# Optimization experiments

Hardware: AMD Instinct MI355X
Metric: run time of the kernel (lower is better)

The kernel has to match this reference:

```python
import jax, jax.numpy as jnp
import numpy as np

NEG_SLOPE = 0.01  # torch F.leaky_relu default

def leaky_relu(z):
    return jnp.where(z >= 0, z, NEG_SLOPE * z)

def setup_inputs() -> dict:
    key = jax.random.key(0)
    k1, k2, k3, k4, k5, k6, k7 = jax.random.split(key, 7)
    n_nodes, d_feat, n_edges, d_edge = 100000, 64, 1000000, 32
    input_dim, hidden_dim = 2 * d_feat + d_edge, 128
    x = jax.random.normal(k1, (n_nodes, d_feat), dtype=jnp.float32)
    edge_index = jax.random.randint(k2, (2, n_edges), 0, n_nodes, dtype=jnp.int64)
    edge_features = jax.random.normal(k3, (n_edges, d_edge), dtype=jnp.float32)
    lim1 = 1.0 / np.sqrt(input_dim)
    W1 = jax.random.uniform(k4, (hidden_dim, input_dim), minval=-lim1, maxval=lim1, dtype=jnp.float32)
    b1 = jax.random.uniform(k5, (hidden_dim,), minval=-lim1, maxval=lim1, dtype=jnp.float32)
    lim2 = 1.0 / np.sqrt(hidden_dim)
    W2 = jax.random.uniform(k6, (1, hidden_dim), minval=-lim2, maxval=lim2, dtype=jnp.float32)
    b2 = jax.random.uniform(k7, (1,), minval=-lim2, maxval=lim2, dtype=jnp.float32)
    return {"x": x, "edge_index": edge_index, "edge_features": edge_features,
            "W1": W1, "b1": b1, "W2": W2, "b2": b2}

def reference(x, edge_index, edge_features, W1, b1, W2, b2):
    origin, destination = edge_index[0], edge_index[1]
    # gather node features per edge and concat: [E, 2*d_feat + d_edge]
    z = jnp.concatenate([x[origin], x[destination], edge_features], axis=1)
    z = leaky_relu(z @ W1.T + b1)   # [E, hidden]
    z = leaky_relu(z @ W2.T + b2)   # [E, 1]
    return z.reshape(-1)
```

## Files before the change

### kernel.cpp

```cpp
#include <hip/hip_runtime.h>
#include <hip/hip_bf16.h>

typedef __attribute__((ext_vector_type(8)))  short          bf16x8;
typedef __attribute__((ext_vector_type(8)))  unsigned short us8;
typedef __attribute__((ext_vector_type(4)))  unsigned short us4;
typedef __attribute__((ext_vector_type(16))) float          f32x16;

static __device__ __forceinline__ unsigned short f2bf(float f) {
    union { float f; unsigned int u; } v; v.f = f;
    unsigned int u = v.u;
    unsigned int r = u + 0x7fffu + ((u >> 16) & 1u);
    return (unsigned short)(r >> 16);
}

static __device__ __forceinline__ bf16x8 pack8(float4 a, float4 b) {
    bf16x8 r;
    r[0] = (short)f2bf(a.x); r[1] = (short)f2bf(a.y);
    r[2] = (short)f2bf(a.z); r[3] = (short)f2bf(a.w);
    r[4] = (short)f2bf(b.x); r[5] = (short)f2bf(b.y);
    r[6] = (short)f2bf(b.z); r[7] = (short)f2bf(b.w);
    return r;
}

__global__ __launch_bounds__(256) void prep_kernel(
    const float* __restrict__ W1, const float* __restrict__ x,
    unsigned short* __restrict__ w1b, unsigned short* __restrict__ xb,
    int nx, int do_x)
{
    if (blockIdx.x == 0) {
        for (int i = threadIdx.x; i < 128 * 160; i += 256)
            w1b[i] = f2bf(W1[i]);
    } else if (do_x) {
        int n4 = nx >> 2;
        int idx = (blockIdx.x - 1) * 256 + threadIdx.x;
        int stride = (gridDim.x - 1) * 256;
        for (int i = idx; i < n4; i += stride) {
            float4 f = ((const float4*)x)[i];
            us4 o = { f2bf(f.x), f2bf(f.y), f2bf(f.z), f2bf(f.w) };
            ((us4*)xb)[i] = o;
        }
    }
}

template <bool XB>
__global__ __launch_bounds__(256) void edge_mlp(
    const float* __restrict__ x, const unsigned short* __restrict__ xb,
    const int* __restrict__ ei, const float* __restrict__ ef,
    const unsigned short* __restrict__ w1b,
    const float* __restrict__ b1, const float* __restrict__ w2,
    const float* __restrict__ b2, float* __restrict__ out, int E)
{
    __shared__ unsigned short W1s[128][168];
    __shared__ float b1s[128];
    __shared__ float w2s[128];

    const int t = threadIdx.x;
    {
        int j = t >> 1, h = t & 1;
        const unsigned short* src = w1b + j * 160 + h * 80;
        unsigned short* dst = &W1s[j][h * 80];
        #pragma unroll
        for (int i = 0; i < 10; i++)
            *(us8*)(dst + i * 8) = *(const us8*)(src + i * 8);
    }
    if (t < 128) { b1s[t] = b1[t]; w2s[t] = w2[t]; }
    __syncthreads();

    const int lane = t & 63;
    const int wv   = t >> 6;
    const int m    = lane & 31;
    const int kg   = lane >> 5;
    const float b2v = b2[0];

    long e = (long)blockIdx.x * 128 + wv * 32 + m;
    int eidx = (int)((e < (long)E) ? e : (long)(E - 1));
    int o = ei[eidx];
    int d = ei[(size_t)E + eidx];

    bf16x8 afrag[10];
    if constexpr (XB) {
        const bf16x8* xo = (const bf16x8*)(xb + (size_t)o * 64 + kg * 8);
        const bf16x8* xd = (const bf16x8*)(xb + (size_t)d * 64 + kg * 8);
        #pragma unroll
        for (int ks = 0; ks < 4; ks++) afrag[ks]     = xo[ks * 2];
        #pragma unroll
        for (int ks = 0; ks < 4; ks++) afrag[4 + ks] = xd[ks * 2];
    } else {
        const float4* xo = (const float4*)(x + (size_t)o * 64 + kg * 8);
        const float4* xd = (const float4*)(x + (size_t)d * 64 + kg * 8);
        #pragma unroll
        for (int ks = 0; ks < 4; ks++) afrag[ks]     = pack8(xo[ks * 4], xo[ks * 4 + 1]);
        #pragma unroll
        for (int ks = 0; ks < 4; ks++) afrag[4 + ks] = pack8(xd[ks * 4], xd[ks * 4 + 1]);
    }
    {
        const float4* pef = (const float4*)(ef + (size_t)eidx * 32 + kg * 8);
        #pragma unroll
        for (int ks = 0; ks < 2; ks++)
            afrag[8 + ks] = pack8(pef[ks * 4], pef[ks * 4 + 1]);
    }

    f32x16 acc[4];
    #pragma unroll
    for (int i = 0; i < 4; i++)
        #pragma unroll
        for (int r = 0; r < 16; r++) acc[i][r] = 0.0f;

    #pragma unroll
    for (int ks = 0; ks < 10; ks++) {
        const int kb = ks * 16 + kg * 8;
        #pragma unroll
        for (int nt = 0; nt < 4; nt++) {
            bf16x8 bfr = *(const bf16x8*)&W1s[nt * 32 + m][kb];
            acc[nt] = __builtin_amdgcn_mfma_f32_32x32x16_bf16(afrag[ks], bfr, acc[nt], 0, 0, 0);
        }
    }

    const int c = m;
    float b1v[4], w2v[4];
    #pragma unroll
    for (int nt = 0; nt < 4; nt++) {
        b1v[nt] = b1s[nt * 32 + c];
        w2v[nt] = w2s[nt * 32 + c];
    }
    float s[16];
    #pragma unroll
    for (int r = 0; r < 16; r++) {
        float a = 0.0f;
        #pragma unroll
        for (int nt = 0; nt < 4; nt++) {
            float h = acc[nt][r] + b1v[nt];
            h = fmaxf(h, 0.01f * h);
            a = fmaf(h, w2v[nt], a);
        }
        s[r] = a;
    }

    #pragma unroll
    for (int k = 0; k < 4; k++) {
        const int msk = 1 << k;
        const int bit = (c >> k) & 1;
        #pragma unroll
        for (int j = 0; j < (8 >> k); j++) {
            float a0 = s[2 * j], a1 = s[2 * j + 1];
            float keep = bit ? a1 : a0;
            float send = bit ? a0 : a1;
            s[j] = keep + __shfl_xor(send, msk, 64);
        }
    }
    float tot = s[0] + __shfl_xor(s[0], 16, 64);

    if ((c & 16) == 0) {
        int row = (c & 3) + 4 * kg + 8 * ((c >> 2) & 3);
        long oidx = (long)blockIdx.x * 128 + wv * 32 + row;
        if (oidx < (long)E) {
            float v = tot + b2v;
            out[oidx] = fmaxf(v, 0.01f * v);
        }
    }
}

extern "C" void kernel_launch(void* const* d_in, const int* in_sizes, int n_in,
                              void* d_out, int out_size, void* d_ws, size_t ws_size,
                              hipStream_t stream)
{
    const float* x  = (const float*)d_in[0];
    const int*   ei = (const int*)d_in[1];
    const float* ef = (const float*)d_in[2];
    const float* W1 = (const float*)d_in[3];
    const float* b1 = (const float*)d_in[4];
    const float* w2 = (const float*)d_in[5];
    const float* b2 = (const float*)d_in[6];
    float* out = (float*)d_out;

    const int E  = in_sizes[1] / 2;
    const int nx = in_sizes[0];

    unsigned short* w1b = (unsigned short*)d_ws;
    unsigned short* xb  = (unsigned short*)((char*)d_ws + 65536);
    const bool use_xb = ws_size >= (size_t)65536 + (size_t)nx * 2;

    const int nblk = (E + 127) / 128;
    prep_kernel<<<use_xb ? 2048 : 1, 256, 0, stream>>>(W1, x, w1b, xb, nx, use_xb ? 1 : 0);
    if (use_xb)
        edge_mlp<true><<<nblk, 256, 0, stream>>>(x, xb, ei, ef, w1b, b1, w2, b2, out, E);
    else
        edge_mlp<false><<<nblk, 256, 0, stream>>>(x, xb, ei, ef, w1b, b1, w2, b2, out, E);
}
```

Baseline: 284.2 us.

## Use persistent grid-stride edge kernel with software-pipelined gathers

Replaces the one-tile-per-block edge MLP with a persistent kernel of 768 blocks that loop over 128-edge tiles. The next tile's node and edge-feature gathers are issued between MFMAs of the current tile, and indices are prefetched two tiles ahead. This is meant to hide gather latency and to amortise the W1 load into shared memory across many tiles. The trade-off is higher register pressure under the launch_bounds(256,3) occupancy target, and a fixed grid size that may not match every CU count.

```diff
diff --git a/kernel.cpp b/kernel.cpp
--- a/kernel.cpp
+++ b/kernel.cpp
@@ -42,9 +42,21 @@
     }
 }
 
-template <bool XB>
-__global__ __launch_bounds__(256) void edge_mlp(
-    const float* __restrict__ x, const unsigned short* __restrict__ xb,
+#define MFMA4(AF, KS)                                                              \
+    {                                                                              \
+        const int kb_ = (KS) * 16 + kg * 8;                                        \
+        acc[0] = __builtin_amdgcn_mfma_f32_32x32x16_bf16(                          \
+            (AF), *(const bf16x8*)&W1s[0 * 32 + m][kb_], acc[0], 0, 0, 0);         \
+        acc[1] = __builtin_amdgcn_mfma_f32_32x32x16_bf16(                          \
+            (AF), *(const bf16x8*)&W1s[1 * 32 + m][kb_], acc[1], 0, 0, 0);         \
+        acc[2] = __builtin_amdgcn_mfma_f32_32x32x16_bf16(                          \
+            (AF), *(const bf16x8*)&W1s[2 * 32 + m][kb_], acc[2], 0, 0, 0);         \
+        acc[3] = __builtin_amdgcn_mfma_f32_32x32x16_bf16(                          \
+            (AF), *(const bf16x8*)&W1s[3 * 32 + m][kb_], acc[3], 0, 0, 0);         \
+    }
+
+__global__ __launch_bounds__(256, 3) void edge_mlp_pers(
+    const unsigned short* __restrict__ xb,
     const int* __restrict__ ei, const float* __restrict__ ef,
     const unsigned short* __restrict__ w1b,
     const float* __restrict__ b1, const float* __restrict__ w2,
@@ -54,6 +66,145 @@
     __shared__ float b1s[128];
     __shared__ float w2s[128];
 
+    const int tid = threadIdx.x;
+    {
+        int j = tid >> 1, h = tid & 1;
+        const unsigned short* src = w1b + j * 160 + h * 80;
+        unsigned short* dst = &W1s[j][h * 80];
+        #pragma unroll
+        for (int i = 0; i < 10; i++)
+            *(us8*)(dst + i * 8) = *(const us8*)(src + i * 8);
+    }
+    if (tid < 128) { b1s[tid] = b1[tid]; w2s[tid] = w2[tid]; }
+    __syncthreads();
+
+    const int lane = tid & 63;
+    const int wv   = tid >> 6;
+    const int m    = lane & 31;
+    const int kg   = lane >> 5;
+    const float b2v = b2[0];
+    const int laneoff = wv * 32 + m;
+
+    float b1v[4], w2v[4];
+    #pragma unroll
+    for (int nt = 0; nt < 4; nt++) {
+        b1v[nt] = b1s[nt * 32 + m];
+        w2v[nt] = w2s[nt * 32 + m];
+    }
+
+    const int ntiles = (E + 127) >> 7;
+    const int NT = gridDim.x;
+    int t = blockIdx.x;
+    if (t >= ntiles) return;
+
+    auto eclamp = [&](int tt) -> int {
+        if (tt >= ntiles) tt = ntiles - 1;
+        long e = (long)tt * 128 + laneoff;
+        return (int)(e < (long)E ? e : (long)(E - 1));
+    };
+
+    const unsigned short* xk = xb + kg * 8;
+
+    int eA = eclamp(t);
+    int oA = ei[eA], dA = ei[(size_t)E + eA];
+    int eB = eclamp(t + NT);
+    int oB = ei[eB], dB = ei[(size_t)E + eB];
+
+    bf16x8 xo[4], xd[4];
+    float4 efr[4];
+    {
+        const bf16x8* po = (const bf16x8*)(xk + (size_t)oA * 64);
+        const bf16x8* pd = (const bf16x8*)(xk + (size_t)dA * 64);
+        #pragma unroll
+        for (int ks = 0; ks < 4; ks++) { xo[ks] = po[ks * 2]; xd[ks] = pd[ks * 2]; }
+        const float4* pe = (const float4*)(ef + (size_t)eA * 32 + kg * 8);
+        efr[0] = pe[0]; efr[1] = pe[1]; efr[2] = pe[4]; efr[3] = pe[5];
+    }
+
+    while (true) {
+        bf16x8 af8 = pack8(efr[0], efr[1]);
+        bf16x8 af9 = pack8(efr[2], efr[3]);
+
+        int eC = eclamp(t + 2 * NT);
+        int oC = ei[eC], dC = ei[(size_t)E + eC];
+
+        f32x16 acc[4];
+        #pragma unroll
+        for (int i = 0; i < 4; i++)
+            #pragma unroll
+            for (int r = 0; r < 16; r++) acc[i][r] = 0.0f;
+
+        const bf16x8* po = (const bf16x8*)(xk + (size_t)oB * 64);
+        const bf16x8* pd = (const bf16x8*)(xk + (size_t)dB * 64);
+        const float4* pe = (const float4*)(ef + (size_t)eB * 32 + kg * 8);
+
+        #pragma unroll
+        for (int ks = 0; ks < 4; ks++) {
+            MFMA4(xo[ks], ks);
+            xo[ks] = po[ks * 2];
+        }
+        #pragma unroll
+        for (int ks = 0; ks < 4; ks++) {
+            MFMA4(xd[ks], ks + 4);
+            xd[ks] = pd[ks * 2];
+        }
+        MFMA4(af8, 8);
+        efr[0] = pe[0]; efr[1] = pe[1];
+        MFMA4(af9, 9);
+        efr[2] = pe[4]; efr[3] = pe[5];
+
+        float s[16];
+        #pragma unroll
+        for (int r = 0; r < 16; r++) {
+            float a = 0.0f;
+            #pragma unroll
+            for (int nt = 0; nt < 4; nt++) {
+                float h = acc[nt][r] + b1v[nt];
+                h = fmaxf(h, 0.01f * h);
+                a = fmaf(h, w2v[nt], a);
+            }
+            s[r] = a;
+        }
+        #pragma unroll
+        for (int k = 0; k < 4; k++) {
+            const int msk = 1 << k;
+            const int bit = (m >> k) & 1;
+            #pragma unroll
+            for (int j = 0; j < (8 >> k); j++) {
+                float a0 = s[2 * j], a1 = s[2 * j + 1];
+                float keep = bit ? a1 : a0;
+                float send = bit ? a0 : a1;
+                s[j] = keep + __shfl_xor(send, msk, 64);
+            }
+        }
+        float tot = s[0] + __shfl_xor(s[0], 16, 64);
+
+        if ((m & 16) == 0) {
+            int row = (m & 3) + 4 * kg + 8 * ((m >> 2) & 3);
+            long oidx = (long)t * 128 + wv * 32 + row;
+            if (oidx < (long)E) {
+                float v = tot + b2v;
+                out[oidx] = fmaxf(v, 0.01f * v);
+            }
+        }
+
+        t += NT;
+        if (t >= ntiles) break;
+        oB = oC; dB = dC; eB = eC;
+    }
+}
+
+__global__ __launch_bounds__(256) void edge_mlp_fb(
+    const float* __restrict__ x,
+    const int* __restrict__ ei, const float* __restrict__ ef,
+    const unsigned short* __restrict__ w1b,
+    const float* __restrict__ b1, const float* __restrict__ w2,
+    const float* __restrict__ b2, float* __restrict__ out, int E)
+{
+    __shared__ unsigned short W1s[128][168];
+    __shared__ float b1s[128];
+    __shared__ float w2s[128];
+
     const int t = threadIdx.x;
     {
         int j = t >> 1, h = t & 1;
@@ -78,22 +229,13 @@
     int d = ei[(size_t)E + eidx];
 
     bf16x8 afrag[10];
-    if constexpr (XB) {
-        const bf16x8* xo = (const bf16x8*)(xb + (size_t)o * 64 + kg * 8);
-        const bf16x8* xd = (const bf16x8*)(xb + (size_t)d * 64 + kg * 8);
-        #pragma unroll
-        for (int ks = 0; ks < 4; ks++) afrag[ks]     = xo[ks * 2];
-        #pragma unroll
-        for (int ks = 0; ks < 4; ks++) afrag[4 + ks] = xd[ks * 2];
-    } else {
+    {
         const float4* xo = (const float4*)(x + (size_t)o * 64 + kg * 8);
         const float4* xd = (const float4*)(x + (size_t)d * 64 + kg * 8);
         #pragma unroll
         for (int ks = 0; ks < 4; ks++) afrag[ks]     = pack8(xo[ks * 4], xo[ks * 4 + 1]);
         #pragma unroll
         for (int ks = 0; ks < 4; ks++) afrag[4 + ks] = pack8(xd[ks * 4], xd[ks * 4 + 1]);
-    }
-    {
         const float4* pef = (const float4*)(ef + (size_t)eidx * 32 + kg * 8);
         #pragma unroll
         for (int ks = 0; ks < 2; ks++)
@@ -108,20 +250,14 @@
 
     #pragma unroll
     for (int ks = 0; ks < 10; ks++) {
-        const int kb = ks * 16 + kg * 8;
-        #pragma unroll
-        for (int nt = 0; nt < 4; nt++) {
-            bf16x8 bfr = *(const bf16x8*)&W1s[nt * 32 + m][kb];
-            acc[nt] = __builtin_amdgcn_mfma_f32_32x32x16_bf16(afrag[ks], bfr, acc[nt], 0, 0, 0);
-        }
-    }
-
-    const int c = m;
+        MFMA4(afrag[ks], ks);
+    }
+
     float b1v[4], w2v[4];
     #pragma unroll
     for (int nt = 0; nt < 4; nt++) {
-        b1v[nt] = b1s[nt * 32 + c];
-        w2v[nt] = w2s[nt * 32 + c];
+        b1v[nt] = b1s[nt * 32 + m];
+        w2v[nt] = w2s[nt * 32 + m];
     }
     float s[16];
     #pragma unroll
@@ -135,11 +271,10 @@
         }
         s[r] = a;
     }
-
     #pragma unroll
     for (int k = 0; k < 4; k++) {
         const int msk = 1 << k;
-        const int bit = (c >> k) & 1;
+        const int bit = (m >> k) & 1;
         #pragma unroll
         for (int j = 0; j < (8 >> k); j++) {
             float a0 = s[2 * j], a1 = s[2 * j + 1];
@@ -150,8 +285,8 @@
     }
     float tot = s[0] + __shfl_xor(s[0], 16, 64);
 
-    if ((c & 16) == 0) {
-        int row = (c & 3) + 4 * kg + 8 * ((c >> 2) & 3);
+    if ((m & 16) == 0) {
+        int row = (m & 3) + 4 * kg + 8 * ((m >> 2) & 3);
         long oidx = (long)blockIdx.x * 128 + wv * 32 + row;
         if (oidx < (long)E) {
             float v = tot + b2v;
@@ -180,10 +315,11 @@
     unsigned short* xb  = (unsigned short*)((char*)d_ws + 65536);
     const bool use_xb = ws_size >= (size_t)65536 + (size_t)nx * 2;
 
-    const int nblk = (E + 127) / 128;
     prep_kernel<<<use_xb ? 2048 : 1, 256, 0, stream>>>(W1, x, w1b, xb, nx, use_xb ? 1 : 0);
-    if (use_xb)
-        edge_mlp<true><<<nblk, 256, 0, stream>>>(x, xb, ei, ef, w1b, b1, w2, b2, out, E);
-    else
-        edge_mlp<false><<<nblk, 256, 0, stream>>>(x, xb, ei, ef, w1b, b1, w2, b2, out, E);
-}
+    if (use_xb) {
+        edge_mlp_pers<<<768, 256, 0, stream>>>(xb, ei, ef, w1b, b1, w2, b2, out, E);
+    } else {
+        const int nblk = (E + 127) / 128;
+        edge_mlp_fb<<<nblk, 256, 0, stream>>>(x, ei, ef, w1b, b1, w2, b2, out, E);
+    }
+}
```

After: 427.3 us. +50.4%, slower.
